# Performance work log

Measured on AMD Instinct MI355X. Metric: run time of the kernel, lower is better.

## Reference

```python
import jax, jax.numpy as jnp
import numpy as np

B, T, E, H = 16, 4096, 64, 8
K, GADD, RADD, REGION = 256, 8, 8, 64
MIN_SIGMA, SIGMA_SCALE, SIGMA_BOOST = 0.05, 1.0, 2.0
VS = K * (4 + GADD + RADD)


def setup_inputs() -> dict:
    key = jax.random.key(0)
    ks = jax.random.split(key, 10)
    return {
        "x": jax.random.normal(ks[0], (B, T, E), jnp.float32),
        "Wq": jax.random.normal(ks[1], (E, E * H), jnp.float32) / np.float32(np.sqrt(E)),
        "Wk": jax.random.normal(ks[2], (E, E * H), jnp.float32) / np.float32(np.sqrt(E)),
        "Wv": jax.random.normal(ks[3], (E, E * H), jnp.float32) / np.float32(np.sqrt(E)),
        "Wu": jax.random.normal(ks[4], (H * E, E), jnp.float32) / np.float32(np.sqrt(H * E)),
        "bu": jnp.zeros((E,), jnp.float32),
        "means_p": jax.random.normal(ks[5], (K, 2), jnp.float32),
        "sigmas_p": jax.random.normal(ks[6], (K,), jnp.float32),
        "global_ints": jax.random.randint(ks[7], (B, 1, K, GADD, 2), 0, T, jnp.int32),
        "local_offsets": jax.random.randint(ks[8], (B, 1, K, RADD, 2), 0, REGION, jnp.int32),
    }


def _flip(x):
    # util.flip: sort each (i, j) pair so row >= col (below-diagonal / causal)
    hi = jnp.max(x, axis=-1, keepdims=True)
    lo = jnp.min(x, axis=-1, keepdims=True)
    return jnp.concatenate([hi, lo], axis=-1)


def _forward(x, Wq, Wk, Wv, Wu, bu, means_p, sigmas_p, global_ints, local_offsets):
    b, t, e = x.shape
    h, k = H, K

    # ---- hyper(): continuous means/sigmas over the (t, t) attention matrix
    means = jnp.broadcast_to(means_p[None, None], (b, 1, k, 2))
    means = _flip(means)
    means = jax.nn.sigmoid(means) * (t - 1)                       # (b,1,k,2) in [0, t-1]
    sig = jax.nn.softplus(sigmas_p + SIGMA_BOOST) + MIN_SIGMA     # (k,)
    sigmas = jnp.broadcast_to((sig * t * SIGMA_SCALE)[None, None, :, None], (b, 1, k, 2))

    # ---- ngenerate: 2^rank floor/ceil neighbours + global + relative-window samples
    fl, ce = jnp.floor(means), jnp.ceil(means)
    pat = jnp.array([[0., 0.], [0., 1.], [1., 0.], [1., 1.]], jnp.float32)  # (4,2)
    neigh = fl[:, :, :, None, :] * (1.0 - pat) + ce[:, :, :, None, :] * pat
    neigh = jnp.clip(neigh, 0, t - 1).astype(jnp.int32)           # (b,1,k,4,2)
    lower = jnp.clip(jnp.floor(means) - REGION // 2, 0, t - REGION).astype(jnp.int32)
    local = lower[:, :, :, None, :] + local_offsets               # (b,1,k,RADD,2)
    idx = jnp.concatenate([neigh, global_ints, local], axis=3).reshape(b, 1, VS, 2)
    idx = _flip(idx)                                              # (b,1,VS,2), row >= col

    # ---- densities: unnormalized Gaussian weight of each int tuple under each point
    indfl = idx.astype(jnp.float32)
    diff = (indfl[:, :, :, None, :] - means[:, :, None, :, :]) / sigmas[:, :, None, :, :]
    props = jnp.exp(-0.5 * jnp.sum(diff * diff, axis=-1))         # (b,1,VS,K)

    # ---- nduplicates: zero all-but-one of identical index tuples per batch
    ids = idx[:, 0, :, 0] * t + idx[:, 0, :, 1]                   # (b, VS)
    def dupmask(v):
        o = jnp.argsort(v)
        s = v[o]
        d = jnp.concatenate([jnp.zeros((1,), bool), s[1:] == s[:-1]])
        return jnp.zeros((VS,), bool).at[o].set(d)
    dups = jax.vmap(dupmask)(ids)                                  # (b, VS)
    props = jnp.where(dups[:, None, :, None], 0.0, props)
    props = props / jnp.sum(props, axis=2, keepdims=True)
    weights = jnp.sum(props, axis=3)                               # mvalues == 1 -> (b,1,VS)

    # ---- Q/K/V projections, per-head dim = e
    scale = e ** -0.25
    q = (x @ Wq).reshape(b, t, h, e).transpose(0, 2, 1, 3).reshape(b * h, t, e) * scale
    kk = (x @ Wk).reshape(b, t, h, e).transpose(0, 2, 1, 3).reshape(b * h, t, e) * scale
    v = (x @ Wv).reshape(b, t, h, e).transpose(0, 2, 1, 3).reshape(b * h, t, e)

    rows = jnp.broadcast_to(idx[:, 0, None, :, 0], (b, h, VS)).reshape(b * h, VS)
    cols = jnp.broadcast_to(idx[:, 0, None, :, 1], (b, h, VS)).reshape(b * h, VS)
    w = jnp.broadcast_to(weights[:, 0, None, :], (b, h, VS)).reshape(b * h, VS)

    sq = jnp.take_along_axis(q, rows[:, :, None], axis=1)          # (b*h, VS, e)
    sk = jnp.take_along_axis(kk, cols[:, :, None], axis=1)
    dot = w * jnp.sum(sq * sk, axis=-1)                            # (b*h, VS)

    # ---- segment (row-wise) softmax over the sparse pattern
    seg = (jnp.arange(b * h, dtype=jnp.int32)[:, None] * t + rows).reshape(-1)
    dflat = dot.reshape(-1)
    m = jax.lax.stop_gradient(jax.ops.segment_max(dflat, seg, num_segments=b * h * t))
    ex = jnp.exp(dflat - m[seg])
    ssum = jax.ops.segment_sum(ex, seg, num_segments=b * h * t)
    p = ex / ssum[seg]                                             # (b*h*VS,)

    # ---- sparse batched matmul: scatter-add p * V[col] into rows
    gathered = jnp.take_along_axis(v, cols[:, :, None], axis=1).reshape(-1, e)
    out = jax.ops.segment_sum(p[:, None] * gathered, seg, num_segments=b * h * t)
    out = out.reshape(b, h, t, e).transpose(0, 2, 1, 3).reshape(b, t, h * e)
    return out @ Wu + bu


def reference(x, Wq, Wk, Wv, Wu, bu, means_p, sigmas_p, global_ints, local_offsets):
    return _forward(x, Wq, Wk, Wv, Wu, bu, means_p, sigmas_p, global_ints, local_offsets)
```

## Files before the change

### kernel.cpp

```cpp
#include <hip/hip_runtime.h>
#include <hip/hip_bf16.h>
#include <math.h>

#define B 16
#define T 4096
#define E 64
#define H 8
#define KP 256
#define GADD 8
#define RADD 8
#define REGION 64
#define VS (KP * (4 + GADD + RADD))
#define NH (H * E)
#define NCHUNK 20
#define HSZ 16384

typedef __attribute__((ext_vector_type(8))) short bf16x8;
typedef __attribute__((ext_vector_type(4))) float f32x4;

__device__ inline ushort f2bf(float f) {
    union { __hip_bfloat16 h; ushort u; } cv;
    cv.h = __float2bfloat16(f);
    return cv.u;
}
__device__ inline float bflo(uint32_t p) { return __uint_as_float(p << 16); }
__device__ inline float bfhi(uint32_t p) { return __uint_as_float(p & 0xffff0000u); }

__global__ void k_points(const float* __restrict__ means_p, const float* __restrict__ sigmas_p,
                         float* __restrict__ meansf, float* __restrict__ sigt) {
    int k = threadIdx.x;
    if (k >= KP) return;
    float a = means_p[2 * k], b = means_p[2 * k + 1];
    float hi = fmaxf(a, b), lo = fminf(a, b);
    meansf[2 * k]     = (1.f / (1.f + expf(-hi))) * (float)(T - 1);
    meansf[2 * k + 1] = (1.f / (1.f + expf(-lo))) * (float)(T - 1);
    float sp = sigmas_p[k] + 2.0f;
    float s = (sp > 20.f) ? sp : log1pf(expf(sp));
    sigt[k] = (s + 0.05f) * (float)T;
}

__global__ void k_wvu(const float* __restrict__ Wv, const float* __restrict__ Wu,
                      float* __restrict__ Wvu) {
    int idx = blockIdx.x * blockDim.x + threadIdx.x;
    if (idx >= E * NH) return;
    int i = idx / NH, c = idx % NH;
    int h = c / E, j = c % E;
    float acc = 0.f;
    for (int d = 0; d < E; ++d)
        acc += Wv[i * NH + h * E + d] * Wu[(h * E + d) * E + j];
    Wvu[i * NH + c] = acc;
}

__global__ void k_prep_x(const float* __restrict__ x, ushort* __restrict__ xb) {
    int i = (blockIdx.x * 256 + threadIdx.x) * 8;
    float4 a = *(const float4*)(x + i);
    float4 b = *(const float4*)(x + i + 4);
    uint4 r;
    r.x = (uint32_t)f2bf(a.x) | ((uint32_t)f2bf(a.y) << 16);
    r.y = (uint32_t)f2bf(a.z) | ((uint32_t)f2bf(a.w) << 16);
    r.z = (uint32_t)f2bf(b.x) | ((uint32_t)f2bf(b.y) << 16);
    r.w = (uint32_t)f2bf(b.z) | ((uint32_t)f2bf(b.w) << 16);
    *(uint4*)(xb + i) = r;
}

__global__ void k_prep_w(const float* __restrict__ Wq, const float* __restrict__ Wk,
                         const float* __restrict__ Wvu, ushort* __restrict__ wfrag) {
    int t = blockIdx.x * 256 + threadIdx.x;
    if (t >= 2 * 32 * 2 * 64) return;
    int lane = t & 63, kf = (t >> 6) & 1, nf = (t >> 7) & 31, z = t >> 12;
    int col = nf * 16 + (lane & 15);
    int krow = kf * 32 + (lane >> 4) * 8;
    uint32_t v[8];
    if (z == 0) {
        int h = col >> 6, d = col & 63;
        const float* wqrow = Wq + (size_t)d * NH + h * 64;
        #pragma unroll
        for (int j = 0; j < 8; ++j) {
            const float* wkrow = Wk + (size_t)(krow + j) * NH + h * 64;
            float acc = 0.f;
            for (int m = 0; m < 64; ++m) acc += wqrow[m] * wkrow[m];
            v[j] = f2bf(acc);
        }
    } else {
        #pragma unroll
        for (int j = 0; j < 8; ++j) v[j] = f2bf(Wvu[(size_t)(krow + j) * NH + col]);
    }
    uint4 r;
    r.x = v[0] | (v[1] << 16); r.y = v[2] | (v[3] << 16);
    r.z = v[4] | (v[5] << 16); r.w = v[6] | (v[7] << 16);
    *(uint4*)(wfrag + (size_t)t * 8) = r;
}

__global__ __launch_bounds__(256) void k_proj(const ushort* __restrict__ xb,
        const ushort* __restrict__ wfrag,
        __hip_bfloat16* __restrict__ xm, __hip_bfloat16* __restrict__ vu) {
    int z = blockIdx.y;
    __hip_bfloat16* outp = (z == 0) ? xm : vu;
    int row0 = blockIdx.x * 64;
    int wv = threadIdx.x >> 6, lane = threadIdx.x & 63;
    int arow = lane & 15, akoff = (lane >> 4) * 8;

    bf16x8 bfr[8][2];
    #pragma unroll
    for (int nf = 0; nf < 8; ++nf) {
        size_t base = ((size_t)((z * 32 + wv * 8 + nf) * 2) * 64 + lane) * 8;
        bfr[nf][0] = *(const bf16x8*)(wfrag + base);
        bfr[nf][1] = *(const bf16x8*)(wfrag + base + 64 * 8);
    }

    #pragma unroll
    for (int mf = 0; mf < 4; ++mf) {
        bf16x8 a0 = *(const bf16x8*)(xb + (size_t)(row0 + mf * 16 + arow) * 64 + akoff);
        bf16x8 a1 = *(const bf16x8*)(xb + (size_t)(row0 + mf * 16 + arow) * 64 + 32 + akoff);
        f32x4 acc[8];
        #pragma unroll
        for (int nf = 0; nf < 8; ++nf) {
            f32x4 t = {0.f, 0.f, 0.f, 0.f};
            t = __builtin_amdgcn_mfma_f32_16x16x32_bf16(a0, bfr[nf][0], t, 0, 0, 0);
            t = __builtin_amdgcn_mfma_f32_16x16x32_bf16(a1, bfr[nf][1], t, 0, 0, 0);
            acc[nf] = t;
        }
        int rbase = row0 + mf * 16 + (lane >> 4) * 4;
        #pragma unroll
        for (int rg = 0; rg < 4; ++rg) {
            uint4 o;
            o.x = (uint32_t)f2bf(acc[0][rg]) | ((uint32_t)f2bf(acc[1][rg]) << 16);
            o.y = (uint32_t)f2bf(acc[2][rg]) | ((uint32_t)f2bf(acc[3][rg]) << 16);
            o.z = (uint32_t)f2bf(acc[4][rg]) | ((uint32_t)f2bf(acc[5][rg]) << 16);
            o.w = (uint32_t)f2bf(acc[6][rg]) | ((uint32_t)f2bf(acc[7][rg]) << 16);
            *(uint4*)((ushort*)outp + (size_t)(rbase + rg) * NH + wv * 128 + (lane & 15) * 8) = o;
        }
    }
}

__global__ void k_build_idx(const int* __restrict__ g_ints, const int* __restrict__ l_offs,
                            const float* __restrict__ meansf,
                            int* __restrict__ idxrow, int* __restrict__ idxcol,
                            int* __restrict__ hkey, int* __restrict__ hval) {
    int b = blockIdx.y;
    int s = blockIdx.x * 256 + threadIdx.x;
    int* keys = hkey + b * HSZ;
    int* vals = hval + b * HSZ;
    int k = s / 20, slot = s % 20;
    float m0 = meansf[2 * k], m1 = meansf[2 * k + 1];
    int i0, i1;
    if (slot < 4) {
        float a  = (slot & 2) ? ceilf(m0) : floorf(m0);
        float bb = (slot & 1) ? ceilf(m1) : floorf(m1);
        a  = fminf(fmaxf(a, 0.f), (float)(T - 1));
        bb = fminf(fmaxf(bb, 0.f), (float)(T - 1));
        i0 = (int)a; i1 = (int)bb;
    } else if (slot < 12) {
        const int* p = g_ints + ((size_t)((b * KP + k) * GADD) + (slot - 4)) * 2;
        i0 = p[0]; i1 = p[1];
    } else {
        int lo0 = (int)fminf(fmaxf(floorf(m0) - (float)(REGION / 2), 0.f), (float)(T - REGION));
        int lo1 = (int)fminf(fmaxf(floorf(m1) - (float)(REGION / 2), 0.f), (float)(T - REGION));
        const int* p = l_offs + ((size_t)((b * KP + k) * RADD) + (slot - 12)) * 2;
        i0 = lo0 + p[0]; i1 = lo1 + p[1];
    }
    int row = max(i0, i1), col = min(i0, i1);
    idxrow[b * VS + s] = row;
    idxcol[b * VS + s] = col;
    int id = row * T + col;
    unsigned h = ((unsigned)id * 2654435761u) >> 18;
    while (true) {
        int old = atomicCAS(&keys[h], -1, id);
        if (old == -1 || old == id) { atomicMin(&vals[h], s); break; }
        h = (h + 1) & (HSZ - 1);
    }
}

__global__ __launch_bounds__(256) void k_local(const int* __restrict__ idxrow,
        const int* __restrict__ idxcol, const int* __restrict__ hkey,
        const int* __restrict__ hval, int* __restrict__ lrank, int* __restrict__ dup,
        int* __restrict__ chist) {
    int b = blockIdx.y, chunk = blockIdx.x;
    int tid = threadIdx.x;
    int s = chunk * 256 + tid;
    int r = idxrow[b * VS + s];
    int c = idxcol[b * VS + s];
    __shared__ int srow[256];
    srow[tid] = r;
    __syncthreads();
    int lr = 0;
    #pragma unroll 8
    for (int t = 0; t < 256; ++t) {
        int rt = srow[t];
        lr += (t < tid && rt == r);
    }
    lrank[b * VS + s] = lr;
    atomicAdd(&chist[(size_t)(b * T + r) * NCHUNK + chunk], 1);
    const int* keys = hkey + b * HSZ;
    const int* vals = hval + b * HSZ;
    int id = r * T + c;
    unsigned h = ((unsigned)id * 2654435761u) >> 18;
    while (keys[h] != id) h = (h + 1) & (HSZ - 1);
    dup[b * VS + s] = (vals[h] != s);
}

__global__ void k_chunkscan(int* __restrict__ chist, int* __restrict__ rowcnt) {
    int idx = blockIdx.x * 256 + threadIdx.x;
    int* p = chist + (size_t)idx * NCHUNK;
    int acc = 0;
    #pragma unroll
    for (int c = 0; c < NCHUNK; ++c) { int v = p[c]; p[c] = acc; acc += v; }
    rowcnt[idx] = acc;
}

__global__ void k_colsum(const int* __restrict__ idxrow, const int* __restrict__ idxcol,
                         const int* __restrict__ dup, const float* __restrict__ meansf,
                         const float* __restrict__ sigt, float* __restrict__ colsum) {
    int k = blockIdx.x, b = blockIdx.y;
    float m0 = meansf[2 * k], m1 = meansf[2 * k + 1];
    float inv = 1.f / sigt[k];
    float acc = 0.f;
    for (int s = threadIdx.x; s < VS; s += 256) {
        if (!dup[b * VS + s]) {
            float d0 = ((float)idxrow[b * VS + s] - m0) * inv;
            float d1 = ((float)idxcol[b * VS + s] - m1) * inv;
            acc += __expf(-0.5f * (d0 * d0 + d1 * d1));
        }
    }
    __shared__ float red[256];
    red[threadIdx.x] = acc;
    __syncthreads();
    for (int o = 128; o > 0; o >>= 1) {
        if (threadIdx.x < o) red[threadIdx.x] += red[threadIdx.x + o];
        __syncthreads();
    }
    if (threadIdx.x == 0) colsum[b * KP + k] = red[0];
}

__global__ void k_weights(const int* __restrict__ idxrow, const int* __restrict__ idxcol,
                          const int* __restrict__ dup, const float* __restrict__ meansf,
                          const float* __restrict__ sigt, const float* __restrict__ colsum,
                          float* __restrict__ wts) {
    int b = blockIdx.y;
    int s = blockIdx.x * 256 + threadIdx.x;
    __shared__ float sm[2 * KP], ss[KP], rc[KP];
    for (int k = threadIdx.x; k < KP; k += 256) {
        sm[2 * k] = meansf[2 * k];
        sm[2 * k + 1] = meansf[2 * k + 1];
        ss[k] = 1.f / sigt[k];
        rc[k] = 1.f / colsum[b * KP + k];
    }
    __syncthreads();
    float w = 0.f;
    if (!dup[b * VS + s]) {
        float r = (float)idxrow[b * VS + s], c = (float)idxcol[b * VS + s];
        #pragma unroll 4
        for (int k = 0; k < KP; ++k) {
            float d0 = (r - sm[2 * k]) * ss[k];
            float d1 = (c - sm[2 * k + 1]) * ss[k];
            w += __expf(-0.5f * (d0 * d0 + d1 * d1)) * rc[k];
        }
    }
    wts[b * VS + s] = w;
}

__global__ __launch_bounds__(1024) void k_scan(const int* __restrict__ rowcnt, int* __restrict__ rowptr) {
    int b = blockIdx.x, tid = threadIdx.x;
    __shared__ int part[1024];
    int v[4]; int loc = 0;
    for (int j = 0; j < 4; ++j) { v[j] = rowcnt[b * T + tid * 4 + j]; loc += v[j]; }
    part[tid] = loc;
    __syncthreads();
    for (int off = 1; off < 1024; off <<= 1) {
        int t = (tid >= off) ? part[tid - off] : 0;
        __syncthreads();
        part[tid] += t;
        __syncthreads();
    }
    int excl = part[tid] - loc;
    for (int j = 0; j < 4; ++j) { rowptr[b * (T + 1) + tid * 4 + j] = excl; excl += v[j]; }
    if (tid == 1023) rowptr[b * (T + 1) + T] = part[1023];
}

__global__ void k_scatter(const int* __restrict__ idxrow, const int* __restrict__ idxcol,
                          const float* __restrict__ wts, const int* __restrict__ lrank,
                          const int* __restrict__ chist, const int* __restrict__ rowptr,
                          int* __restrict__ scol, float* __restrict__ sw) {
    int b = blockIdx.y;
    int s = blockIdx.x * 256 + threadIdx.x;
    int r = idxrow[b * VS + s];
    int pos = rowptr[b * (T + 1) + r] + chist[(size_t)(b * T + r) * NCHUNK + (s >> 8)]
            + lrank[b * VS + s];
    scol[b * VS + pos] = idxcol[b * VS + s];
    sw[b * VS + pos] = wts[b * VS + s];
}

__global__ __launch_bounds__(256) void k_attn(
        const float* __restrict__ x, const __hip_bfloat16* __restrict__ xm,
        const __hip_bfloat16* __restrict__ vu, const int* __restrict__ rowptr,
        const int* __restrict__ scol, const float* __restrict__ sw,
        const float* __restrict__ bu, float* __restrict__ out) {
    int gr = blockIdx.x * 4 + (threadIdx.x >> 6);
    int b = gr >> 12;
    int r = gr & (T - 1);
    int lane = threadIdx.x & 63;
    int p0 = rowptr[b * (T + 1) + r], p1 = rowptr[b * (T + 1) + r + 1];

    const float* xrow = x + (size_t)gr * E + (lane & 15);
    float xv0 = xrow[0], xv1 = xrow[16], xv2 = xrow[32], xv3 = xrow[48];

    float m0 = -INFINITY, s0 = 0.f, m1 = -INFINITY, s1 = 0.f;
    float av[8] = {0.f,0.f,0.f,0.f,0.f,0.f,0.f,0.f};

    for (int e = p0; e < p1; ++e) {
        int c = scol[b * VS + e];
        float w = sw[b * VS + e];
        size_t off = ((size_t)(b * T + c)) * NH + lane * 8;
        uint4 k4 = *(const uint4*)((const ushort*)xm + off);
        float dp0 = xv0*bflo(k4.x) + xv1*bfhi(k4.x) + xv2*bflo(k4.y) + xv3*bfhi(k4.y);
        float dp1 = xv0*bflo(k4.z) + xv1*bfhi(k4.z) + xv2*bflo(k4.w) + xv3*bfhi(k4.w);
        dp0 += __shfl_xor(dp0, 1);
        dp0 += __shfl_xor(dp0, 2);
        dp0 += __shfl_xor(dp0, 4);
        dp0 += __shfl_xor(dp0, 8);
        dp1 += __shfl_xor(dp1, 1);
        dp1 += __shfl_xor(dp1, 2);
        dp1 += __shfl_xor(dp1, 4);
        dp1 += __shfl_xor(dp1, 8);
        float d0 = 0.125f * w * dp0;
        float d1 = 0.125f * w * dp1;
        uint4 v4 = *(const uint4*)((const ushort*)vu + off);
        float vf[8] = { bflo(v4.x), bfhi(v4.x), bflo(v4.y), bfhi(v4.y),
                        bflo(v4.z), bfhi(v4.z), bflo(v4.w), bfhi(v4.w) };
        float nm0 = fmaxf(m0, d0), c0 = __expf(m0 - nm0), t0 = __expf(d0 - nm0);
        float nm1 = fmaxf(m1, d1), c1 = __expf(m1 - nm1), t1 = __expf(d1 - nm1);
        s0 = s0 * c0 + t0; m0 = nm0;
        s1 = s1 * c1 + t1; m1 = nm1;
        #pragma unroll
        for (int u = 0; u < 4; ++u) av[u] = av[u] * c0 + t0 * vf[u];
        #pragma unroll
        for (int u = 4; u < 8; ++u) av[u] = av[u] * c1 + t1 * vf[u];
    }

    float i0 = (p1 > p0) ? (1.f / s0) : 0.f;
    float i1 = (p1 > p0) ? (1.f / s1) : 0.f;
    float res[4];
    #pragma unroll
    for (int u = 0; u < 4; ++u) {
        float v = av[u] * i0 + av[u + 4] * i1;
        v += __shfl_xor(v, 16);
        v += __shfl_xor(v, 32);
        res[u] = v;
    }
    if (lane < 16) {
        #pragma unroll
        for (int u = 0; u < 4; ++u)
            out[(size_t)gr * E + u * 16 + lane] = res[u] + bu[u * 16 + lane];
    }
}

extern "C" void kernel_launch(void* const* d_in, const int* in_sizes, int n_in,
                              void* d_out, int out_size, void* d_ws, size_t ws_size,
                              hipStream_t stream) {
    const float* x        = (const float*)d_in[0];
    const float* Wq       = (const float*)d_in[1];
    const float* Wk       = (const float*)d_in[2];
    const float* Wv       = (const float*)d_in[3];
    const float* Wu       = (const float*)d_in[4];
    const float* bu       = (const float*)d_in[5];
    const float* means_p  = (const float*)d_in[6];
    const float* sigmas_p = (const float*)d_in[7];
    const int*   g_ints   = (const int*)d_in[8];
    const int*   l_offs   = (const int*)d_in[9];
    float* out = (float*)d_out;

    char* ws = (char*)d_ws;
    size_t o = 0;
    auto alloc = [&](size_t bytes) -> void* {
        void* p = ws + o;
        o += (bytes + 255) & ~(size_t)255;
        return p;
    };
    __hip_bfloat16* xm  = (__hip_bfloat16*)alloc((size_t)B * T * NH * 2);
    __hip_bfloat16* vu  = (__hip_bfloat16*)alloc((size_t)B * T * NH * 2);
    ushort* xb    = (ushort*)alloc((size_t)B * T * E * 2);
    ushort* wfrag = (ushort*)alloc((size_t)2 * 32 * 2 * 64 * 8 * 2);
    float* Wvu    = (float*)alloc((size_t)E * NH * 4);
    float* meansf = (float*)alloc(KP * 2 * 4);
    float* sigt   = (float*)alloc(KP * 4);
    int*   idxrow = (int*)alloc((size_t)B * VS * 4);
    int*   idxcol = (int*)alloc((size_t)B * VS * 4);
    float* wts    = (float*)alloc((size_t)B * VS * 4);
    int*   lrank  = (int*)alloc((size_t)B * VS * 4);
    int*   dup    = (int*)alloc((size_t)B * VS * 4);
    float* colsum = (float*)alloc((size_t)B * KP * 4);
    int*   rowcnt = (int*)alloc((size_t)B * T * 4);
    int*   rowptr = (int*)alloc((size_t)B * (T + 1) * 4);
    int*   scol   = (int*)alloc((size_t)B * VS * 4);
    float* sw     = (float*)alloc((size_t)B * VS * 4);
    int*   hkey   = (int*)alloc((size_t)B * HSZ * 4);
    int*   hval   = (int*)alloc((size_t)B * HSZ * 4);
    int*   chist  = (int*)alloc((size_t)B * T * NCHUNK * 4);

    hipMemsetAsync(hkey, 0xFF, (size_t)B * HSZ * 4, stream);
    hipMemsetAsync(hval, 0x7F, (size_t)B * HSZ * 4, stream);
    hipMemsetAsync(chist, 0, (size_t)B * T * NCHUNK * 4, stream);

    k_points<<<1, 256, 0, stream>>>(means_p, sigmas_p, meansf, sigt);
    k_wvu<<<(E * NH + 255) / 256, 256, 0, stream>>>(Wv, Wu, Wvu);
    k_prep_x<<<(B * T * E / 8) / 256, 256, 0, stream>>>(x, xb);
    k_prep_w<<<(2 * 32 * 2 * 64 + 255) / 256, 256, 0, stream>>>(Wq, Wk, Wvu, wfrag);
    k_build_idx<<<dim3(VS / 256, B), 256, 0, stream>>>(g_ints, l_offs, meansf, idxrow, idxcol, hkey, hval);
    k_local<<<dim3(NCHUNK, B), 256, 0, stream>>>(idxrow, idxcol, hkey, hval, lrank, dup, chist);
    k_chunkscan<<<B * T / 256, 256, 0, stream>>>(chist, rowcnt);
    k_colsum<<<dim3(KP, B), 256, 0, stream>>>(idxrow, idxcol, dup, meansf, sigt, colsum);
    k_weights<<<dim3(VS / 256, B), 256, 0, stream>>>(idxrow, idxcol, dup, meansf, sigt, colsum, wts);
    k_scan<<<B, 1024, 0, stream>>>(rowcnt, rowptr);
    k_scatter<<<dim3(VS / 256, B), 256, 0, stream>>>(idxrow, idxcol, wts, lrank, chist, rowptr, scol, sw);
    k_proj<<<dim3(B * T / 64, 2), 256, 0, stream>>>(xb, wfrag, xm, vu);
    k_attn<<<B * T / 4, 256, 0, stream>>>(x, xm, vu, rowptr, scol, sw, bu, out);
}
```

Before: 188.8 us.

## Fuse prep kernels, memsets and chunk scan; pack col/weight; swizzle attention blocks

Merges the point, Wvu, x-conversion and weight-fragment kernels into one launch. The Wv·Wu product is now computed inline per fragment. The three memsets become one init kernel, and the per-row chunk prefix is folded into the row scan kernel. Column indices and weights are packed into an int2 array so the attention loop does one load per edge. Attention blocks are swizzled across batches. The aim is to cut launch overhead and memory traffic, at the cost of a longer serial chunk scan inside k_scan (only 16 blocks) and redundant Wv·Wu work.

New measurement: 194.3 us. 1.03x slower.

```diff
diff --git a/kernel.cpp b/kernel.cpp
--- a/kernel.cpp
+++ b/kernel.cpp
@@ -26,69 +26,73 @@
 __device__ inline float bflo(uint32_t p) { return __uint_as_float(p << 16); }
 __device__ inline float bfhi(uint32_t p) { return __uint_as_float(p & 0xffff0000u); }
 
-__global__ void k_points(const float* __restrict__ means_p, const float* __restrict__ sigmas_p,
-                         float* __restrict__ meansf, float* __restrict__ sigt) {
-    int k = threadIdx.x;
-    if (k >= KP) return;
-    float a = means_p[2 * k], b = means_p[2 * k + 1];
-    float hi = fmaxf(a, b), lo = fminf(a, b);
-    meansf[2 * k]     = (1.f / (1.f + expf(-hi))) * (float)(T - 1);
-    meansf[2 * k + 1] = (1.f / (1.f + expf(-lo))) * (float)(T - 1);
-    float sp = sigmas_p[k] + 2.0f;
-    float s = (sp > 20.f) ? sp : log1pf(expf(sp));
-    sigt[k] = (s + 0.05f) * (float)T;
-}
-
-__global__ void k_wvu(const float* __restrict__ Wv, const float* __restrict__ Wu,
-                      float* __restrict__ Wvu) {
-    int idx = blockIdx.x * blockDim.x + threadIdx.x;
-    if (idx >= E * NH) return;
-    int i = idx / NH, c = idx % NH;
-    int h = c / E, j = c % E;
-    float acc = 0.f;
-    for (int d = 0; d < E; ++d)
-        acc += Wv[i * NH + h * E + d] * Wu[(h * E + d) * E + j];
-    Wvu[i * NH + c] = acc;
-}
-
-__global__ void k_prep_x(const float* __restrict__ x, ushort* __restrict__ xb) {
-    int i = (blockIdx.x * 256 + threadIdx.x) * 8;
-    float4 a = *(const float4*)(x + i);
-    float4 b = *(const float4*)(x + i + 4);
-    uint4 r;
-    r.x = (uint32_t)f2bf(a.x) | ((uint32_t)f2bf(a.y) << 16);
-    r.y = (uint32_t)f2bf(a.z) | ((uint32_t)f2bf(a.w) << 16);
-    r.z = (uint32_t)f2bf(b.x) | ((uint32_t)f2bf(b.y) << 16);
-    r.w = (uint32_t)f2bf(b.z) | ((uint32_t)f2bf(b.w) << 16);
-    *(uint4*)(xb + i) = r;
-}
-
-__global__ void k_prep_w(const float* __restrict__ Wq, const float* __restrict__ Wk,
-                         const float* __restrict__ Wvu, ushort* __restrict__ wfrag) {
-    int t = blockIdx.x * 256 + threadIdx.x;
-    if (t >= 2 * 32 * 2 * 64) return;
-    int lane = t & 63, kf = (t >> 6) & 1, nf = (t >> 7) & 31, z = t >> 12;
-    int col = nf * 16 + (lane & 15);
-    int krow = kf * 32 + (lane >> 4) * 8;
-    uint32_t v[8];
-    if (z == 0) {
-        int h = col >> 6, d = col & 63;
-        const float* wqrow = Wq + (size_t)d * NH + h * 64;
-        #pragma unroll
-        for (int j = 0; j < 8; ++j) {
-            const float* wkrow = Wk + (size_t)(krow + j) * NH + h * 64;
-            float acc = 0.f;
-            for (int m = 0; m < 64; ++m) acc += wqrow[m] * wkrow[m];
-            v[j] = f2bf(acc);
+__global__ void k_init(int* __restrict__ hkey, int* __restrict__ hval, int* __restrict__ chist) {
+    int i = blockIdx.x * 256 + threadIdx.x;
+    hkey[i] = -1;
+    hval[i] = 0x7fffffff;
+    #pragma unroll
+    for (int j = 0; j < 5; ++j) chist[i + j * (B * HSZ)] = 0;
+}
+
+__global__ void k_prep(const float* __restrict__ x,
+                       const float* __restrict__ Wq, const float* __restrict__ Wk,
+                       const float* __restrict__ Wv, const float* __restrict__ Wu,
+                       const float* __restrict__ means_p, const float* __restrict__ sigmas_p,
+                       ushort* __restrict__ xb, ushort* __restrict__ wfrag,
+                       float* __restrict__ meansf, float* __restrict__ sigt) {
+    int bid = blockIdx.x, tid = threadIdx.x;
+    if (bid < 32) {
+        int t = bid * 256 + tid;
+        int lane = t & 63, kf = (t >> 6) & 1, nf = (t >> 7) & 31, z = t >> 12;
+        int col = nf * 16 + (lane & 15);
+        int krow = kf * 32 + (lane >> 4) * 8;
+        int h = col >> 6, jc = col & 63;
+        uint32_t v[8];
+        if (z == 0) {
+            const float* wqrow = Wq + (size_t)jc * NH + h * 64;
+            #pragma unroll
+            for (int j = 0; j < 8; ++j) {
+                const float* wkrow = Wk + (size_t)(krow + j) * NH + h * 64;
+                float acc = 0.f;
+                for (int m = 0; m < 64; ++m) acc += wqrow[m] * wkrow[m];
+                v[j] = f2bf(acc);
+            }
+        } else {
+            #pragma unroll
+            for (int j = 0; j < 8; ++j) {
+                const float* wvrow = Wv + (size_t)(krow + j) * NH + h * 64;
+                const float* wucol = Wu + (size_t)h * 64 * 64 + jc;
+                float acc = 0.f;
+                for (int d = 0; d < 64; ++d) acc += wvrow[d] * wucol[d * 64];
+                v[j] = f2bf(acc);
+            }
+        }
+        uint4 r;
+        r.x = v[0] | (v[1] << 16); r.y = v[2] | (v[3] << 16);
+        r.z = v[4] | (v[5] << 16); r.w = v[6] | (v[7] << 16);
+        *(uint4*)(wfrag + (size_t)t * 8) = r;
+    } else if (bid == 32) {
+        int k = tid;
+        if (k < KP) {
+            float a = means_p[2 * k], b = means_p[2 * k + 1];
+            float hi = fmaxf(a, b), lo = fminf(a, b);
+            meansf[2 * k]     = (1.f / (1.f + expf(-hi))) * (float)(T - 1);
+            meansf[2 * k + 1] = (1.f / (1.f + expf(-lo))) * (float)(T - 1);
+            float sp = sigmas_p[k] + 2.0f;
+            float s = (sp > 20.f) ? sp : log1pf(expf(sp));
+            sigt[k] = (s + 0.05f) * (float)T;
         }
     } else {
-        #pragma unroll
-        for (int j = 0; j < 8; ++j) v[j] = f2bf(Wvu[(size_t)(krow + j) * NH + col]);
-    }
-    uint4 r;
-    r.x = v[0] | (v[1] << 16); r.y = v[2] | (v[3] << 16);
-    r.z = v[4] | (v[5] << 16); r.w = v[6] | (v[7] << 16);
-    *(uint4*)(wfrag + (size_t)t * 8) = r;
+        int i = ((bid - 33) * 256 + tid) * 8;
+        float4 a = *(const float4*)(x + i);
+        float4 b = *(const float4*)(x + i + 4);
+        uint4 r;
+        r.x = (uint32_t)f2bf(a.x) | ((uint32_t)f2bf(a.y) << 16);
+        r.y = (uint32_t)f2bf(a.z) | ((uint32_t)f2bf(a.w) << 16);
+        r.z = (uint32_t)f2bf(b.x) | ((uint32_t)f2bf(b.y) << 16);
+        r.w = (uint32_t)f2bf(b.z) | ((uint32_t)f2bf(b.w) << 16);
+        *(uint4*)(xb + i) = r;
+    }
 }
 
 __global__ __launch_bounds__(256) void k_proj(const ushort* __restrict__ xb,
@@ -199,15 +203,6 @@
     dup[b * VS + s] = (vals[h] != s);
 }
 
-__global__ void k_chunkscan(int* __restrict__ chist, int* __restrict__ rowcnt) {
-    int idx = blockIdx.x * 256 + threadIdx.x;
-    int* p = chist + (size_t)idx * NCHUNK;
-    int acc = 0;
-    #pragma unroll
-    for (int c = 0; c < NCHUNK; ++c) { int v = p[c]; p[c] = acc; acc += v; }
-    rowcnt[idx] = acc;
-}
-
 __global__ void k_colsum(const int* __restrict__ idxrow, const int* __restrict__ idxcol,
                          const int* __restrict__ dup, const float* __restrict__ meansf,
                          const float* __restrict__ sigt, float* __restrict__ colsum) {
@@ -259,11 +254,19 @@
     wts[b * VS + s] = w;
 }
 
-__global__ __launch_bounds__(1024) void k_scan(const int* __restrict__ rowcnt, int* __restrict__ rowptr) {
+__global__ __launch_bounds__(1024) void k_scan(int* __restrict__ chist, int* __restrict__ rowptr) {
     int b = blockIdx.x, tid = threadIdx.x;
     __shared__ int part[1024];
     int v[4]; int loc = 0;
-    for (int j = 0; j < 4; ++j) { v[j] = rowcnt[b * T + tid * 4 + j]; loc += v[j]; }
+    #pragma unroll
+    for (int j = 0; j < 4; ++j) {
+        int row = tid * 4 + j;
+        int* p = chist + (size_t)(b * T + row) * NCHUNK;
+        int acc = 0;
+        #pragma unroll
+        for (int c = 0; c < NCHUNK; ++c) { int t = p[c]; p[c] = acc; acc += t; }
+        v[j] = acc; loc += acc;
+    }
     part[tid] = loc;
     __syncthreads();
     for (int off = 1; off < 1024; off <<= 1) {
@@ -273,6 +276,7 @@
         __syncthreads();
     }
     int excl = part[tid] - loc;
+    #pragma unroll
     for (int j = 0; j < 4; ++j) { rowptr[b * (T + 1) + tid * 4 + j] = excl; excl += v[j]; }
     if (tid == 1023) rowptr[b * (T + 1) + T] = part[1023];
 }
@@ -280,22 +284,23 @@
 __global__ void k_scatter(const int* __restrict__ idxrow, const int* __restrict__ idxcol,
                           const float* __restrict__ wts, const int* __restrict__ lrank,
                           const int* __restrict__ chist, const int* __restrict__ rowptr,
-                          int* __restrict__ scol, float* __restrict__ sw) {
+                          int2* __restrict__ scw) {
     int b = blockIdx.y;
     int s = blockIdx.x * 256 + threadIdx.x;
     int r = idxrow[b * VS + s];
     int pos = rowptr[b * (T + 1) + r] + chist[(size_t)(b * T + r) * NCHUNK + (s >> 8)]
             + lrank[b * VS + s];
-    scol[b * VS + pos] = idxcol[b * VS + s];
-    sw[b * VS + pos] = wts[b * VS + s];
+    scw[b * VS + pos] = make_int2(idxcol[b * VS + s], __float_as_int(wts[b * VS + s]));
 }
 
 __global__ __launch_bounds__(256) void k_attn(
         const float* __restrict__ x, const __hip_bfloat16* __restrict__ xm,
         const __hip_bfloat16* __restrict__ vu, const int* __restrict__ rowptr,
-        const int* __restrict__ scol, const float* __restrict__ sw,
-        const float* __restrict__ bu, float* __restrict__ out) {
-    int gr = blockIdx.x * 4 + (threadIdx.x >> 6);
+        const int2* __restrict__ scw, const float* __restrict__ bu,
+        float* __restrict__ out) {
+    int bid = blockIdx.x;
+    int swz = ((bid & 7) << 11) | (bid >> 3);
+    int gr = swz * 4 + (threadIdx.x >> 6);
     int b = gr >> 12;
     int r = gr & (T - 1);
     int lane = threadIdx.x & 63;
@@ -308,8 +313,9 @@
     float av[8] = {0.f,0.f,0.f,0.f,0.f,0.f,0.f,0.f};
 
     for (int e = p0; e < p1; ++e) {
-        int c = scol[b * VS + e];
-        float w = sw[b * VS + e];
+        int2 ew = scw[b * VS + e];
+        int c = ew.x;
+        float w = __int_as_float(ew.y);
         size_t off = ((size_t)(b * T + c)) * NH + lane * 8;
         uint4 k4 = *(const uint4*)((const ushort*)xm + off);
         float dp0 = xv0*bflo(k4.x) + xv1*bfhi(k4.x) + xv2*bflo(k4.y) + xv3*bfhi(k4.y);
@@ -380,7 +386,6 @@
     __hip_bfloat16* vu  = (__hip_bfloat16*)alloc((size_t)B * T * NH * 2);
     ushort* xb    = (ushort*)alloc((size_t)B * T * E * 2);
     ushort* wfrag = (ushort*)alloc((size_t)2 * 32 * 2 * 64 * 8 * 2);
-    float* Wvu    = (float*)alloc((size_t)E * NH * 4);
     float* meansf = (float*)alloc(KP * 2 * 4);
     float* sigt   = (float*)alloc(KP * 4);
     int*   idxrow = (int*)alloc((size_t)B * VS * 4);
@@ -389,29 +394,21 @@
     int*   lrank  = (int*)alloc((size_t)B * VS * 4);
     int*   dup    = (int*)alloc((size_t)B * VS * 4);
     float* colsum = (float*)alloc((size_t)B * KP * 4);
-    int*   rowcnt = (int*)alloc((size_t)B * T * 4);
     int*   rowptr = (int*)alloc((size_t)B * (T + 1) * 4);
-    int*   scol   = (int*)alloc((size_t)B * VS * 4);
-    float* sw     = (float*)alloc((size_t)B * VS * 4);
+    int2*  scw    = (int2*)alloc((size_t)B * VS * 8);
     int*   hkey   = (int*)alloc((size_t)B * HSZ * 4);
     int*   hval   = (int*)alloc((size_t)B * HSZ * 4);
     int*   chist  = (int*)alloc((size_t)B * T * NCHUNK * 4);
 
-    hipMemsetAsync(hkey, 0xFF, (size_t)B * HSZ * 4, stream);
-    hipMemsetAsync(hval, 0x7F, (size_t)B * HSZ * 4, stream);
-    hipMemsetAsync(chist, 0, (size_t)B * T * NCHUNK * 4, stream);
-
-    k_points<<<1, 256, 0, stream>>>(means_p, sigmas_p, meansf, sigt);
-    k_wvu<<<(E * NH + 255) / 256, 256, 0, stream>>>(Wv, Wu, Wvu);
-    k_prep_x<<<(B * T * E / 8) / 256, 256, 0, stream>>>(x, xb);
-    k_prep_w<<<(2 * 32 * 2 * 64 + 255) / 256, 256, 0, stream>>>(Wq, Wk, Wvu, wfrag);
+    k_init<<<B * HSZ / 256, 256, 0, stream>>>(hkey, hval, chist);
+    k_prep<<<33 + (B * T * E / 8) / 256, 256, 0, stream>>>(x, Wq, Wk, Wv, Wu,
+            means_p, sigmas_p, xb, wfrag, meansf, sigt);
     k_build_idx<<<dim3(VS / 256, B), 256, 0, stream>>>(g_ints, l_offs, meansf, idxrow, idxcol, hkey, hval);
     k_local<<<dim3(NCHUNK, B), 256, 0, stream>>>(idxrow, idxcol, hkey, hval, lrank, dup, chist);
-    k_chunkscan<<<B * T / 256, 256, 0, stream>>>(chist, rowcnt);
     k_colsum<<<dim3(KP, B), 256, 0, stream>>>(idxrow, idxcol, dup, meansf, sigt, colsum);
     k_weights<<<dim3(VS / 256, B), 256, 0, stream>>>(idxrow, idxcol, dup, meansf, sigt, colsum, wts);
-    k_scan<<<B, 1024, 0, stream>>>(rowcnt, rowptr);
-    k_scatter<<<dim3(VS / 256, B), 256, 0, stream>>>(idxrow, idxcol, wts, lrank, chist, rowptr, scol, sw);
+    k_scan<<<B, 1024, 0, stream>>>(chist, rowptr);
+    k_scatter<<<dim3(VS / 256, B), 256, 0, stream>>>(idxrow, idxcol, wts, lrank, chist, rowptr, scw);
     k_proj<<<dim3(B * T / 64, 2), 256, 0, stream>>>(xb, wfrag, xm, vu);
-    k_attn<<<B * T / 4, 256, 0, stream>>>(x, xm, vu, rowptr, scol, sw, bu, out);
-}
+    k_attn<<<B * T / 4, 256, 0, stream>>>(x, xm, vu, rowptr, scw, bu, out);
+}
```
